# Kernel tuning notes

Hardware: AMD Instinct MI355X
Metric: run time of the kernel (lower is better)

Reference implementation:

```python
import jax, jax.numpy as jnp
import numpy as np

N_NODES = 50000
N_EDGES = 1600000
N_GRAPHS = 1000


def setup_inputs() -> dict:
    key = jax.random.key(0)
    ks = jax.random.split(key, 16)
    s = 0.1
    return {
        "x": jax.random.normal(ks[0], (N_NODES, 7), jnp.float32),
        "edge_attr": jax.random.normal(ks[1], (N_EDGES, 4), jnp.float32),
        "edge_index": jax.random.randint(ks[2], (2, N_EDGES), 0, N_NODES),
        "batch": jnp.sort(jax.random.randint(ks[3], (N_NODES,), 0, N_GRAPHS)),
        "We1": jax.random.normal(ks[4], (4, 7), jnp.float32) * s,
        "be1": jnp.zeros((7,), jnp.float32),
        "W1a": jax.random.normal(ks[5], (7, 64), jnp.float32) * s,
        "b1a": jnp.zeros((64,), jnp.float32),
        "W1b": jax.random.normal(ks[6], (64, 64), jnp.float32) * s,
        "b1b": jnp.zeros((64,), jnp.float32),
        "We2": jax.random.normal(ks[7], (4, 64), jnp.float32) * s,
        "be2": jnp.zeros((64,), jnp.float32),
        "W2a": jax.random.normal(ks[8], (64, 64), jnp.float32) * s,
        "b2a": jnp.zeros((64,), jnp.float32),
        "W2b": jax.random.normal(ks[9], (64, 64), jnp.float32) * s,
        "b2b": jnp.zeros((64,), jnp.float32),
        "Wfc": jax.random.normal(ks[10], (64, 12), jnp.float32) * s,
        "bfc": jnp.zeros((12,), jnp.float32),
    }


def _gine_conv(h, edge_attr, src, dst, We, be, Wa, ba, Wb, bb, n_nodes):
    # GINEConv (eps=0): out = nn(h + sum_j relu(h[src] + lin(edge_attr)))
    e = edge_attr @ We + be                      # [E, d]
    msg = jax.nn.relu(h[src] + e)                # [E, d] gather + add + relu
    aggr = jax.ops.segment_sum(msg, dst, num_segments=n_nodes)  # scatter-sum
    z = h + aggr
    return jax.nn.relu(z @ Wa + ba) @ Wb + bb


def reference(x, edge_attr, edge_index, batch,
              We1, be1, W1a, b1a, W1b, b1b,
              We2, be2, W2a, b2a, W2b, b2b,
              Wfc, bfc):
    src, dst = edge_index[0], edge_index[1]
    n = x.shape[0]
    h = jax.nn.relu(_gine_conv(x, edge_attr, src, dst, We1, be1, W1a, b1a, W1b, b1b, n))
    h = jax.nn.relu(_gine_conv(h, edge_attr, src, dst, We2, be2, W2a, b2a, W2b, b2b, n))
    # global mean pool over batch index
    sums = jax.ops.segment_sum(h, batch, num_segments=N_GRAPHS)          # [G, 64]
    cnt = jax.ops.segment_sum(jnp.ones((n,), h.dtype), batch, num_segments=N_GRAPHS)
    pooled = sums / jnp.maximum(cnt, 1.0)[:, None]
    return pooled @ Wfc + bfc                                            # [G, 12]
```

## Files before the change

kernel.cpp:

```cpp
#include <hip/hip_runtime.h>

typedef unsigned char uchar;
typedef unsigned short ushort;
typedef unsigned int uint;

constexpr int NN = 50000;
constexpr int NE = 1600000;
constexpr int NG = 1000;
constexpr int NB2 = 196;
constexpr int TILE = 4096;
constexpr int NTILE = (NE + TILE - 1) / TILE;
constexpr int SPAN_CAP = 9216;
constexpr int MSTRIDE = 72;

constexpr int OFF_BCNT  = 0;
constexpr int OFF_SUMS  = 256;
constexpr int OFF_CNT   = 64256;
constexpr int ZERO_UNITS= 65280;
constexpr int OFF_BBASE = 65280;
constexpr int OFF_BCUR  = 65536;
constexpr int OFF_OFFS  = 65792;
constexpr int OFF_P0    = 116224;
constexpr int OFF_P1    = 1716224;
constexpr int OFF_P2    = 3316224;
constexpr int OFF_Z1    = 4916224;
constexpr int OFF_H1    = 5316224;
constexpr int OFF_Z     = 6916224;

typedef __attribute__((ext_vector_type(8))) short short8;
typedef __attribute__((ext_vector_type(4))) float float4v;
typedef __attribute__((ext_vector_type(2))) float float2v;

__device__ __forceinline__ uint f2bf(float f) {
    uint u = __float_as_uint(f);
    return (u + 0x7fffu + ((u >> 16) & 1u)) >> 16;
}
__device__ __forceinline__ float bf2f_lo(uint p) { return __uint_as_float(p << 16); }
__device__ __forceinline__ float bf2f_hi(uint p) { return __uint_as_float(p & 0xffff0000u); }

__global__ __launch_bounds__(256) void bhist_kernel(const int* __restrict__ eidx,
                                                    int* __restrict__ bcnt) {
    __shared__ int lh[NB2];
    for (int i = threadIdx.x; i < NB2; i += 256) lh[i] = 0;
    __syncthreads();
    int tid = blockIdx.x * 256 + threadIdx.x;
    int stride = gridDim.x * 256;
    for (int e = tid; e < NE; e += stride) atomicAdd(&lh[eidx[NE + e] >> 8], 1);
    __syncthreads();
    for (int i = threadIdx.x; i < NB2; i += 256) if (lh[i]) atomicAdd(&bcnt[i], lh[i]);
}

__global__ __launch_bounds__(256) void bscan_kernel(const int* __restrict__ bcnt,
                                                    int* __restrict__ bbase,
                                                    int* __restrict__ bcur) {
    __shared__ int s[256];
    int t = threadIdx.x;
    int v = (t < NB2) ? bcnt[t] : 0;
    s[t] = v; __syncthreads();
    for (int o = 1; o < 256; o <<= 1) {
        int u = (t >= o) ? s[t - o] : 0;
        __syncthreads();
        s[t] += u;
        __syncthreads();
    }
    bbase[t] = s[t] - v;
    bcur[t] = s[t] - v;
}

__global__ __launch_bounds__(256) void bin_kernel(const int* __restrict__ eidx,
                                                  const float4* __restrict__ ea,
                                                  int* __restrict__ bcur,
                                                  uint* __restrict__ p0,
                                                  uint* __restrict__ p1,
                                                  uint* __restrict__ p2) {
    __shared__ uint s0[TILE], s1[TILE], s2[TILE];
    __shared__ int hcnt[NB2], hoff[NB2 + 1], hcur[NB2], gbase[NB2];
    const int t = threadIdx.x;
    const int e0 = blockIdx.x * TILE;
    const int cnt = (NE - e0 < TILE) ? (NE - e0) : TILE;
    for (int i = t; i < NB2; i += 256) hcnt[i] = 0;
    __syncthreads();
    int dsts[16];
    #pragma unroll
    for (int k = 0; k < 16; ++k) {
        int i = t + k * 256;
        int d = (i < cnt) ? eidx[NE + e0 + i] : -1;
        dsts[k] = d;
        if (d >= 0) atomicAdd(&hcnt[d >> 8], 1);
    }
    __syncthreads();
    if (t == 0) {
        int a = 0;
        for (int b = 0; b < NB2; ++b) { hoff[b] = a; a += hcnt[b]; }
        hoff[NB2] = a;
    }
    __syncthreads();
    if (t < NB2) { hcur[t] = hoff[t]; gbase[t] = atomicAdd(&bcur[t], hcnt[t]); }
    __syncthreads();
    #pragma unroll
    for (int k = 0; k < 16; ++k) {
        int d = dsts[k];
        if (d < 0) continue;
        int i = t + k * 256;
        int e = e0 + i;
        int src = eidx[e];
        float4 a = ea[e];
        int bkt = d >> 8;
        int lp = atomicAdd(&hcur[bkt], 1);
        s0[lp] = (uint)src | ((uint)(d & 255) << 16) | ((uint)bkt << 24);
        s1[lp] = f2bf(a.x) | (f2bf(a.y) << 16);
        s2[lp] = f2bf(a.z) | (f2bf(a.w) << 16);
    }
    __syncthreads();
    for (int i = t; i < cnt; i += 256) {
        uint r0 = s0[i];
        int bkt = (int)(r0 >> 24);
        int gp = gbase[bkt] + (i - hoff[bkt]);
        p0[gp] = r0; p1[gp] = s1[i]; p2[gp] = s2[i];
    }
}

__global__ __launch_bounds__(256) void build_kernel(const int* __restrict__ bbase,
                                                    const int* __restrict__ bcnt,
                                                    int* __restrict__ offs,
                                                    uint* __restrict__ p0,
                                                    uint* __restrict__ p1,
                                                    uint* __restrict__ p2) {
    __shared__ uint s0[SPAN_CAP], s1[SPAN_CAP], s2[SPAN_CAP];
    __shared__ int ldeg[256], lcur[256], sscan[256];
    const int t = threadIdx.x;
    const int b = blockIdx.x;
    const int nlo = b << 8;
    const int base = bbase[b];
    int span = bcnt[b];
    if (span > SPAN_CAP) span = SPAN_CAP;
    ldeg[t] = 0;
    __syncthreads();
    for (int i = t; i < span; i += 256)
        atomicAdd(&ldeg[(p0[base + i] >> 16) & 0xFFu], 1);
    __syncthreads();
    int v = ldeg[t];
    sscan[t] = v; __syncthreads();
    for (int o = 1; o < 256; o <<= 1) {
        int u = (t >= o) ? sscan[t - o] : 0;
        __syncthreads();
        sscan[t] += u;
        __syncthreads();
    }
    int exc = sscan[t] - v;
    lcur[t] = exc;
    int gi = nlo + t;
    if (gi < NN) offs[gi] = base + exc;
    else if (gi < 50176) offs[gi] = NE;
    __syncthreads();
    for (int i = t; i < span; i += 256) {
        uint r0 = p0[base + i], r1 = p1[base + i], r2 = p2[base + i];
        int pos = atomicAdd(&lcur[(r0 >> 16) & 0xFFu], 1);
        s0[pos] = r0; s1[pos] = r1; s2[pos] = r2;
    }
    __syncthreads();
    for (int i = t; i < span; i += 256) {
        p0[base + i] = s0[i]; p1[base + i] = s1[i]; p2[base + i] = s2[i];
    }
}

__global__ __launch_bounds__(256) void aggr1_kernel(
    const float* __restrict__ x,
    const uint* __restrict__ p0, const uint* __restrict__ p1, const uint* __restrict__ p2,
    const int* __restrict__ offs,
    const float* __restrict__ We1, const float* __restrict__ be1,
    float* __restrict__ z1)
{
    __shared__ float sWe[32];
    __shared__ float sbe[8];
    int tid = threadIdx.x;
    if (tid < 32) { int k = tid >> 3, dd = tid & 7; sWe[tid] = (dd < 7) ? We1[k * 7 + dd] : 0.f; }
    if (tid < 8)  sbe[tid] = (tid < 7) ? be1[tid] : 0.f;
    __syncthreads();

    const int w = tid >> 6, lane = tid & 63;
    const int jg = lane >> 3, d = lane & 7;

    for (int n = blockIdx.x * 4 + w; n < NN; n += gridDim.x * 4) {
        const int off = offs[n];
        const int deg = offs[n + 1] - off;
        float acc = 0.f;
        for (int j0 = 0; j0 < deg; j0 += 16) {
            int ja = j0 + jg;
            int jb = j0 + 8 + jg;
            int ia = off + ((ja < deg) ? ja : 0);
            int ib = off + ((jb < deg) ? jb : 0);
            uint r0a = p0[ia], r1a = p1[ia], r2a = p2[ia];
            uint r0b = p0[ib], r1b = p1[ib], r2b = p2[ib];
            float xa = (d < 7) ? x[(size_t)(r0a & 0xFFFFu) * 7 + d] : 0.f;
            float xb = (d < 7) ? x[(size_t)(r0b & 0xFFFFu) * 7 + d] : 0.f;
            float va = sbe[d] + bf2f_lo(r1a) * sWe[d] + bf2f_hi(r1a) * sWe[8 + d]
                     + bf2f_lo(r2a) * sWe[16 + d] + bf2f_hi(r2a) * sWe[24 + d] + xa;
            float vb = sbe[d] + bf2f_lo(r1b) * sWe[d] + bf2f_hi(r1b) * sWe[8 + d]
                     + bf2f_lo(r2b) * sWe[16 + d] + bf2f_hi(r2b) * sWe[24 + d] + xb;
            va = (d < 7 && ja < deg) ? fmaxf(va, 0.f) : 0.f;
            vb = (d < 7 && jb < deg) ? fmaxf(vb, 0.f) : 0.f;
            acc += va + vb;
        }
        acc += __shfl_xor(acc, 8);
        acc += __shfl_xor(acc, 16);
        acc += __shfl_xor(acc, 32);
        if (jg == 0)
            z1[(size_t)n * 8 + d] = (d < 7) ? (x[(size_t)n * 7 + d] + acc) : 0.f;
    }
}

__global__ __launch_bounds__(256) void node1_kernel(
    const float* __restrict__ z1,
    const float* __restrict__ W1a, const float* __restrict__ b1a,
    const float* __restrict__ W1b, const float* __restrict__ b1b,
    uint* __restrict__ h1u)
{
    __shared__ __align__(16) ushort sT[64 * MSTRIDE];
    __shared__ __align__(16) ushort sO[64 * 64];
    const int t = threadIdx.x;
    const int w = t >> 6, lane = t & 63;
    const int qm = lane & 15, quad = lane >> 4;
    const int n0 = blockIdx.x * 64;
    const int node = n0 + w * 16 + qm;

    short8 wa1n[4];
    #pragma unroll
    for (int nt = 0; nt < 4; ++nt) {
        short8 v = (short8)0;
        if (quad == 0) {
            #pragma unroll
            for (int j = 0; j < 7; ++j)
                v[j] = (short)f2bf(W1a[j * 64 + nt * 16 + qm]);
        }
        wa1n[nt] = v;
    }
    short8 wb1[2][4];
    #pragma unroll
    for (int s = 0; s < 2; ++s)
        #pragma unroll
        for (int nt = 0; nt < 4; ++nt) {
            short8 v;
            #pragma unroll
            for (int j = 0; j < 8; ++j)
                v[j] = (short)f2bf(W1b[(s * 32 + quad * 8 + j) * 64 + nt * 16 + qm]);
            wb1[s][nt] = v;
        }
    float ba[4], bb[4];
    #pragma unroll
    for (int nt = 0; nt < 4; ++nt) { ba[nt] = b1a[nt * 16 + qm]; bb[nt] = b1b[nt * 16 + qm]; }

    short8 af1 = (short8)0;
    if (quad == 0 && node < NN) {
        const float4 za = *(const float4*)(z1 + (size_t)node * 8);
        const float4 zbv = *(const float4*)(z1 + (size_t)node * 8 + 4);
        af1[0] = (short)f2bf(za.x); af1[1] = (short)f2bf(za.y);
        af1[2] = (short)f2bf(za.z); af1[3] = (short)f2bf(za.w);
        af1[4] = (short)f2bf(zbv.x); af1[5] = (short)f2bf(zbv.y);
        af1[6] = (short)f2bf(zbv.z); af1[7] = (short)f2bf(zbv.w);
    }
    float4v acc[4];
    #pragma unroll
    for (int nt = 0; nt < 4; ++nt) {
        acc[nt] = (float4v){0.f, 0.f, 0.f, 0.f};
        acc[nt] = __builtin_amdgcn_mfma_f32_16x16x32_bf16(af1, wa1n[nt], acc[nt], 0, 0, 0);
    }
    #pragma unroll
    for (int nt = 0; nt < 4; ++nt)
        #pragma unroll
        for (int r = 0; r < 4; ++r)
            sT[(w * 16 + quad * 4 + r) * MSTRIDE + nt * 16 + qm] =
                (ushort)f2bf(fmaxf(acc[nt][r] + ba[nt], 0.f));
    __syncthreads();

    #pragma unroll
    for (int nt = 0; nt < 4; ++nt) acc[nt] = (float4v){0.f, 0.f, 0.f, 0.f};
    #pragma unroll
    for (int s = 0; s < 2; ++s) {
        short8 af = *(const short8*)&sT[(w * 16 + qm) * MSTRIDE + s * 32 + quad * 8];
        #pragma unroll
        for (int nt = 0; nt < 4; ++nt)
            acc[nt] = __builtin_amdgcn_mfma_f32_16x16x32_bf16(af, wb1[s][nt], acc[nt], 0, 0, 0);
    }
    #pragma unroll
    for (int nt = 0; nt < 4; ++nt)
        #pragma unroll
        for (int r = 0; r < 4; ++r)
            sO[(w * 16 + quad * 4 + r) * 64 + nt * 16 + qm] =
                (ushort)f2bf(fmaxf(acc[nt][r] + bb[nt], 0.f));
    __syncthreads();
    for (int i = t; i < 64 * 32; i += 256) {
        int nd = i >> 5;
        if (n0 + nd < NN) h1u[(size_t)(n0 + nd) * 32 + (i & 31)] = ((const uint*)sO)[i];
    }
}

__global__ __launch_bounds__(256) void aggr2_kernel(
    const uint* __restrict__ h1u,
    const uint* __restrict__ p0, const uint* __restrict__ p1, const uint* __restrict__ p2,
    const int* __restrict__ offs,
    const float* __restrict__ We2, const float* __restrict__ be2,
    uint* __restrict__ zb)
{
    __shared__ float sWe[256];
    __shared__ float sbe[64];
    int tid = threadIdx.x;
    sWe[tid] = We2[tid];
    if (tid < 64) sbe[tid] = be2[tid];
    __syncthreads();
    const int w = tid >> 6, lane = tid & 63;
    const int l = lane & 31;
    const int half8 = (lane >> 5) << 3;
    const int n = blockIdx.x * 4 + w;
    const int off = offs[n];
    const int deg = offs[n + 1] - off;
    float2v w0v, w1v, w2v, w3v, bbv;
    w0v[0] = sWe[2 * l];       w0v[1] = sWe[2 * l + 1];
    w1v[0] = sWe[64 + 2 * l];  w1v[1] = sWe[64 + 2 * l + 1];
    w2v[0] = sWe[128 + 2 * l]; w2v[1] = sWe[128 + 2 * l + 1];
    w3v[0] = sWe[192 + 2 * l]; w3v[1] = sWe[192 + 2 * l + 1];
    bbv[0] = sbe[2 * l];       bbv[1] = sbe[2 * l + 1];
    const float2v zero2 = {0.f, 0.f};

    float2v accv = zero2;
    for (int jb = 0; jb < deg; jb += 16) {
        int m = deg - jb;
        int ll = (lane < 16) ? ((lane < m) ? lane : 0) : 0;
        int idx = off + jb + ll;
        int sx = (int)(p0[idx] & 0xFFFFu);
        uint e01 = p1[idx];
        uint e23 = p2[idx];
        uint g[8];
        #pragma unroll
        for (int k = 0; k < 8; ++k) {
            int mk = k + half8;
            int sk = __shfl(sx, (mk < m) ? mk : 0);
            g[k] = h1u[(size_t)sk * 32 + l];
        }
        #pragma unroll
        for (int k = 0; k < 8; ++k) {
            int mk = k + half8;
            int sl = (mk < m) ? mk : 0;
            uint py = (uint)__shfl((int)e01, sl);
            uint pz = (uint)__shfl((int)e23, sl);
            float2v bv = bbv + bf2f_lo(py) * w0v + bf2f_hi(py) * w1v
                       + bf2f_lo(pz) * w2v + bf2f_hi(pz) * w3v;
            float2v gv;
            gv[0] = bf2f_lo(g[k]);
            gv[1] = bf2f_hi(g[k]);
            float2v tv = gv + bv;
            tv[0] = fmaxf(tv[0], 0.f);
            tv[1] = fmaxf(tv[1], 0.f);
            if (mk < m) accv += tv;
        }
    }
    float accx = accv[0], accy = accv[1];
    accx += __shfl_xor(accx, 32);
    accy += __shfl_xor(accy, 32);
    if (lane < 32) {
        uint sw = h1u[(size_t)n * 32 + l];
        float zx = bf2f_lo(sw) + accx;
        float zy = bf2f_hi(sw) + accy;
        zb[(size_t)n * 32 + l] = f2bf(zx) | (f2bf(zy) << 16);
    }
}

__global__ __launch_bounds__(256) void mlp2_kernel(
    const uint* __restrict__ zb,
    const float* __restrict__ W2a, const float* __restrict__ b2a,
    const float* __restrict__ W2b, const float* __restrict__ b2b,
    const int* __restrict__ batch,
    float* __restrict__ sums, float* __restrict__ cnt)
{
    __shared__ __align__(16) ushort sT[64 * MSTRIDE];
    __shared__ float sH[64 * 64];
    __shared__ int sB[64];
    __shared__ float pbuf[4][64];
    __shared__ int pcnt[4];
    const int t = threadIdx.x;
    const int w = t >> 6, lane = t & 63;
    const int qm = lane & 15, quad = lane >> 4;
    const int n0 = blockIdx.x * 64;
    const int node = n0 + w * 16 + qm;
    const int nv = (NN - n0 < 64) ? (NN - n0) : 64;

    if (t < 64) sB[t] = (n0 + t < NN) ? batch[n0 + t] : -2;

    short8 wa[2][4], wb[2][4];
    #pragma unroll
    for (int s = 0; s < 2; ++s)
        #pragma unroll
        for (int nt = 0; nt < 4; ++nt) {
            short8 va, vb;
            #pragma unroll
            for (int j = 0; j < 8; ++j) {
                int k = s * 32 + quad * 8 + j, n = nt * 16 + qm;
                va[j] = (short)f2bf(W2a[k * 64 + n]);
                vb[j] = (short)f2bf(W2b[k * 64 + n]);
            }
            wa[s][nt] = va; wb[s][nt] = vb;
        }
    float ba[4], bb[4];
    #pragma unroll
    for (int nt = 0; nt < 4; ++nt) { ba[nt] = b2a[nt * 16 + qm]; bb[nt] = b2b[nt * 16 + qm]; }

    float4v acc[4];
    #pragma unroll
    for (int nt = 0; nt < 4; ++nt) acc[nt] = (float4v){0.f, 0.f, 0.f, 0.f};
    #pragma unroll
    for (int s = 0; s < 2; ++s) {
        uint4 zw = (node < NN) ? *(const uint4*)&zb[(size_t)node * 32 + s * 16 + quad * 4]
                               : make_uint4(0, 0, 0, 0);
        short8 af;
        *(uint4*)&af = zw;
        #pragma unroll
        for (int nt = 0; nt < 4; ++nt)
            acc[nt] = __builtin_amdgcn_mfma_f32_16x16x32_bf16(af, wa[s][nt], acc[nt], 0, 0, 0);
    }
    #pragma unroll
    for (int nt = 0; nt < 4; ++nt)
        #pragma unroll
        for (int r = 0; r < 4; ++r)
            sT[(w * 16 + quad * 4 + r) * MSTRIDE + nt * 16 + qm] =
                (ushort)f2bf(fmaxf(acc[nt][r] + ba[nt], 0.f));
    __syncthreads();

    #pragma unroll
    for (int nt = 0; nt < 4; ++nt) acc[nt] = (float4v){0.f, 0.f, 0.f, 0.f};
    #pragma unroll
    for (int s = 0; s < 2; ++s) {
        short8 af = *(const short8*)&sT[(w * 16 + qm) * MSTRIDE + s * 32 + quad * 8];
        #pragma unroll
        for (int nt = 0; nt < 4; ++nt)
            acc[nt] = __builtin_amdgcn_mfma_f32_16x16x32_bf16(af, wb[s][nt], acc[nt], 0, 0, 0);
    }
    #pragma unroll
    for (int nt = 0; nt < 4; ++nt)
        #pragma unroll
        for (int r = 0; r < 4; ++r)
            sH[(w * 16 + quad * 4 + r) * 64 + nt * 16 + qm] = fmaxf(acc[nt][r] + bb[nt], 0.f);
    __syncthreads();

    const int glo = sB[0];
    const int ghi = sB[nv - 1];
    const int c = t >> 6, d = t & 63;
    for (int g = glo; g <= ghi; ++g) {
        float p = 0.f;
        int lc = 0;
        #pragma unroll 4
        for (int i = 0; i < 16; ++i) {
            int nd = c * 16 + i;
            if (sB[nd] == g) { p += sH[nd * 64 + d]; ++lc; }
        }
        pbuf[c][d] = p;
        if (d == 0) pcnt[c] = lc;
        __syncthreads();
        int tc = pcnt[0] + pcnt[1] + pcnt[2] + pcnt[3];
        if (tc > 0) {
            if (c == 0) {
                float tot = pbuf[0][d] + pbuf[1][d] + pbuf[2][d] + pbuf[3][d];
                atomicAdd(&sums[(size_t)g * 64 + d], tot);
            }
            if (t == 0) atomicAdd(&cnt[g], (float)tc);
        }
        __syncthreads();
    }
}

__global__ __launch_bounds__(256) void fc_kernel(
    const float* __restrict__ sums, const float* __restrict__ cnt,
    const float* __restrict__ Wfc, const float* __restrict__ bfc,
    float* __restrict__ out)
{
    int gid = blockIdx.x * blockDim.x + threadIdx.x;
    if (gid >= NG * 12) return;
    int g = gid / 12, jj = gid - g * 12;
    float inv = 1.f / fmaxf(cnt[g], 1.f);
    float acc = bfc[jj];
    #pragma unroll 8
    for (int k = 0; k < 64; ++k) acc += sums[(size_t)g * 64 + k] * inv * Wfc[k * 12 + jj];
    out[gid] = acc;
}

extern "C" void kernel_launch(void* const* d_in, const int* in_sizes, int n_in,
                              void* d_out, int out_size, void* d_ws, size_t ws_size,
                              hipStream_t stream)
{
    (void)in_sizes; (void)n_in; (void)out_size; (void)ws_size;
    const float*  x    = (const float*)d_in[0];
    const float4* ea   = (const float4*)d_in[1];
    const int*    eidx = (const int*)d_in[2];
    const int*    batch= (const int*)d_in[3];
    const float*  We1  = (const float*)d_in[4];
    const float*  be1  = (const float*)d_in[5];
    const float*  W1a  = (const float*)d_in[6];
    const float*  b1a  = (const float*)d_in[7];
    const float*  W1b  = (const float*)d_in[8];
    const float*  b1b  = (const float*)d_in[9];
    const float*  We2  = (const float*)d_in[10];
    const float*  be2  = (const float*)d_in[11];
    const float*  W2a  = (const float*)d_in[12];
    const float*  b2a  = (const float*)d_in[13];
    const float*  W2b  = (const float*)d_in[14];
    const float*  b2b  = (const float*)d_in[15];
    const float*  Wfc  = (const float*)d_in[16];
    const float*  bfc  = (const float*)d_in[17];
    float* out = (float*)d_out;
    float* ws  = (float*)d_ws;

    int*   bcnt  = (int*)(ws + OFF_BCNT);
    float* sums  = ws + OFF_SUMS;
    float* cnt   = ws + OFF_CNT;
    int*   bbase = (int*)(ws + OFF_BBASE);
    int*   bcur  = (int*)(ws + OFF_BCUR);
    int*   offs  = (int*)(ws + OFF_OFFS);
    uint*  p0    = (uint*)(ws + OFF_P0);
    uint*  p1    = (uint*)(ws + OFF_P1);
    uint*  p2    = (uint*)(ws + OFF_P2);
    float* z1    = ws + OFF_Z1;
    uint*  h1u   = (uint*)(ws + OFF_H1);
    uint*  zb    = (uint*)(ws + OFF_Z);

    hipMemsetAsync(d_ws, 0, (size_t)ZERO_UNITS * 4, stream);

    bhist_kernel<<<256, 256, 0, stream>>>(eidx, bcnt);
    bscan_kernel<<<1, 256, 0, stream>>>(bcnt, bbase, bcur);
    bin_kernel  <<<NTILE, 256, 0, stream>>>(eidx, ea, bcur, p0, p1, p2);
    build_kernel<<<NB2, 256, 0, stream>>>(bbase, bcnt, offs, p0, p1, p2);
    aggr1_kernel<<<2500, 256, 0, stream>>>(x, p0, p1, p2, offs, We1, be1, z1);
    node1_kernel<<<(NN + 63) / 64, 256, 0, stream>>>(z1, W1a, b1a, W1b, b1b, h1u);
    aggr2_kernel<<<12500, 256, 0, stream>>>(h1u, p0, p1, p2, offs, We2, be2, zb);
    mlp2_kernel <<<(NN + 63) / 64, 256, 0, stream>>>(zb, W2a, b2a, W2b, b2b, batch, sums, cnt);
    fc_kernel   <<<(NG * 12 + 255) / 256, 256, 0, stream>>>(sums, cnt, Wfc, bfc, out);
}
```

Baseline: 280.0 us.

## Aggregate layer-2 edges per 32-node group with shared-memory atomics

The second aggregation kernel moves from one wavefront per destination node to one block per 32 consecutive nodes. Each half-wavefront handles an edge slot across the group's contiguous CSR edge range and accumulates into a shared-memory tile with atomic adds, using the dst low byte stored in p0. This removes the per-node degree-loop imbalance and the shuffle-heavy broadcast, which leaves lanes idle on low-degree nodes. In exchange it adds LDS atomic contention, depends on the packed dst-local field, and may index past offs when the last group is partial.

```diff
diff --git a/kernel.cpp b/kernel.cpp
--- a/kernel.cpp
+++ b/kernel.cpp
@@ -12,6 +12,8 @@
 constexpr int NTILE = (NE + TILE - 1) / TILE;
 constexpr int SPAN_CAP = 9216;
 constexpr int MSTRIDE = 72;
+constexpr int GRP = 32;
+constexpr int NGB = (NN + GRP - 1) / GRP;
 
 constexpr int OFF_BCNT  = 0;
 constexpr int OFF_SUMS  = 256;
@@ -304,64 +306,78 @@
 {
     __shared__ float sWe[256];
     __shared__ float sbe[64];
-    int tid = threadIdx.x;
+    __shared__ float sAcc[GRP][64];
+    const int tid = threadIdx.x;
     sWe[tid] = We2[tid];
     if (tid < 64) sbe[tid] = be2[tid];
-    __syncthreads();
-    const int w = tid >> 6, lane = tid & 63;
+    {
+        float* sa = &sAcc[0][0];
+        #pragma unroll
+        for (int i = tid; i < GRP * 64; i += 256) sa[i] = 0.f;
+    }
+    __syncthreads();
+
+    const int lane = tid & 63;
     const int l = lane & 31;
-    const int half8 = (lane >> 5) << 3;
-    const int n = blockIdx.x * 4 + w;
-    const int off = offs[n];
-    const int deg = offs[n + 1] - off;
+    const int hh = tid >> 5;
+    const int n0 = blockIdx.x * GRP;
+    const int estart = offs[n0];
+    const int eend = offs[n0 + GRP];
+    const int baseloc = n0 & 255;
+
     float2v w0v, w1v, w2v, w3v, bbv;
     w0v[0] = sWe[2 * l];       w0v[1] = sWe[2 * l + 1];
     w1v[0] = sWe[64 + 2 * l];  w1v[1] = sWe[64 + 2 * l + 1];
     w2v[0] = sWe[128 + 2 * l]; w2v[1] = sWe[128 + 2 * l + 1];
     w3v[0] = sWe[192 + 2 * l]; w3v[1] = sWe[192 + 2 * l + 1];
     bbv[0] = sbe[2 * l];       bbv[1] = sbe[2 * l + 1];
-    const float2v zero2 = {0.f, 0.f};
-
-    float2v accv = zero2;
-    for (int jb = 0; jb < deg; jb += 16) {
-        int m = deg - jb;
-        int ll = (lane < 16) ? ((lane < m) ? lane : 0) : 0;
-        int idx = off + jb + ll;
-        int sx = (int)(p0[idx] & 0xFFFFu);
-        uint e01 = p1[idx];
-        uint e23 = p2[idx];
-        uint g[8];
-        #pragma unroll
-        for (int k = 0; k < 8; ++k) {
-            int mk = k + half8;
-            int sk = __shfl(sx, (mk < m) ? mk : 0);
-            g[k] = h1u[(size_t)sk * 32 + l];
-        }
-        #pragma unroll
-        for (int k = 0; k < 8; ++k) {
-            int mk = k + half8;
-            int sl = (mk < m) ? mk : 0;
-            uint py = (uint)__shfl((int)e01, sl);
-            uint pz = (uint)__shfl((int)e23, sl);
-            float2v bv = bbv + bf2f_lo(py) * w0v + bf2f_hi(py) * w1v
-                       + bf2f_lo(pz) * w2v + bf2f_hi(pz) * w3v;
-            float2v gv;
-            gv[0] = bf2f_lo(g[k]);
-            gv[1] = bf2f_hi(g[k]);
-            float2v tv = gv + bv;
-            tv[0] = fmaxf(tv[0], 0.f);
-            tv[1] = fmaxf(tv[1], 0.f);
-            if (mk < m) accv += tv;
-        }
-    }
-    float accx = accv[0], accy = accv[1];
-    accx += __shfl_xor(accx, 32);
-    accy += __shfl_xor(accy, 32);
-    if (lane < 32) {
-        uint sw = h1u[(size_t)n * 32 + l];
-        float zx = bf2f_lo(sw) + accx;
-        float zy = bf2f_hi(sw) + accy;
-        zb[(size_t)n * 32 + l] = f2bf(zx) | (f2bf(zy) << 16);
+
+    int e = estart + hh;
+    for (; e + 24 < eend; e += 32) {
+        uint r0[4], ry[4], rz[4];
+        #pragma unroll
+        for (int k = 0; k < 4; ++k) {
+            r0[k] = p0[e + 8 * k];
+            ry[k] = p1[e + 8 * k];
+            rz[k] = p2[e + 8 * k];
+        }
+        uint g[4];
+        #pragma unroll
+        for (int k = 0; k < 4; ++k)
+            g[k] = h1u[((r0[k] & 0xFFFFu) << 5) + l];
+        #pragma unroll
+        for (int k = 0; k < 4; ++k) {
+            float2v bv = bbv + bf2f_lo(ry[k]) * w0v + bf2f_hi(ry[k]) * w1v
+                       + bf2f_lo(rz[k]) * w2v + bf2f_hi(rz[k]) * w3v;
+            float t0 = fmaxf(bf2f_lo(g[k]) + bv[0], 0.f);
+            float t1 = fmaxf(bf2f_hi(g[k]) + bv[1], 0.f);
+            int loc = (int)((r0[k] >> 16) & 0xFFu) - baseloc;
+            atomicAdd(&sAcc[loc][l], t0);
+            atomicAdd(&sAcc[loc][32 + l], t1);
+        }
+    }
+    for (; e < eend; e += 8) {
+        uint r0 = p0[e], ry = p1[e], rz = p2[e];
+        uint g = h1u[((r0 & 0xFFFFu) << 5) + l];
+        float2v bv = bbv + bf2f_lo(ry) * w0v + bf2f_hi(ry) * w1v
+                   + bf2f_lo(rz) * w2v + bf2f_hi(rz) * w3v;
+        float t0 = fmaxf(bf2f_lo(g) + bv[0], 0.f);
+        float t1 = fmaxf(bf2f_hi(g) + bv[1], 0.f);
+        int loc = (int)((r0 >> 16) & 0xFFu) - baseloc;
+        atomicAdd(&sAcc[loc][l], t0);
+        atomicAdd(&sAcc[loc][32 + l], t1);
+    }
+    __syncthreads();
+
+    for (int i = tid; i < GRP * 32; i += 256) {
+        int ndl = i >> 5, c = i & 31;
+        int nd = n0 + ndl;
+        if (nd < NN) {
+            uint sw = h1u[(size_t)nd * 32 + c];
+            float zx = bf2f_lo(sw) + sAcc[ndl][c];
+            float zy = bf2f_hi(sw) + sAcc[ndl][32 + c];
+            zb[(size_t)nd * 32 + c] = f2bf(zx) | (f2bf(zy) << 16);
+        }
     }
 }
 
@@ -529,7 +545,7 @@
     build_kernel<<<NB2, 256, 0, stream>>>(bbase, bcnt, offs, p0, p1, p2);
     aggr1_kernel<<<2500, 256, 0, stream>>>(x, p0, p1, p2, offs, We1, be1, z1);
     node1_kernel<<<(NN + 63) / 64, 256, 0, stream>>>(z1, W1a, b1a, W1b, b1b, h1u);
-    aggr2_kernel<<<12500, 256, 0, stream>>>(h1u, p0, p1, p2, offs, We2, be2, zb);
+    aggr2_kernel<<<NGB, 256, 0, stream>>>(h1u, p0, p1, p2, offs, We2, be2, zb);
     mlp2_kernel <<<(NN + 63) / 64, 256, 0, stream>>>(zb, W2a, b2a, W2b, b2b, batch, sums, cnt);
     fc_kernel   <<<(NG * 12 + 255) / 256, 256, 0, stream>>>(sums, cnt, Wfc, bfc, out);
 }
```

New measurement: 823.3 us. +194.0%, slower.

## Remap aggr2 to four nodes per wavefront with 16-lane groups and uint2 gathers

Applied to the files above, without the earlier changes.

Layer-2 aggregation now gives each 16-lane group its own destination node, so one wavefront handles four nodes instead of one. Each lane covers four features through 8-byte gathers, edges are processed two at a time, and the edge-weight vectors are loaded straight from global memory rather than staged in shared memory. This removes the shuffle broadcasts, the shared-memory barrier and the 16-edge batch padding. In exchange, every group loops to the largest degree among the four nodes in its wave, and each lane issues its own edge-record loads, which are redundant across the group.

```diff
diff --git a/kernel.cpp b/kernel.cpp
--- a/kernel.cpp
+++ b/kernel.cpp
@@ -12,6 +12,8 @@
 constexpr int NTILE = (NE + TILE - 1) / TILE;
 constexpr int SPAN_CAP = 9216;
 constexpr int MSTRIDE = 72;
+constexpr int NPB = 16;
+constexpr int NBLK2 = NN / NPB;
 
 constexpr int OFF_BCNT  = 0;
 constexpr int OFF_SUMS  = 256;
@@ -302,67 +304,95 @@
     const float* __restrict__ We2, const float* __restrict__ be2,
     uint* __restrict__ zb)
 {
-    __shared__ float sWe[256];
-    __shared__ float sbe[64];
-    int tid = threadIdx.x;
-    sWe[tid] = We2[tid];
-    if (tid < 64) sbe[tid] = be2[tid];
-    __syncthreads();
-    const int w = tid >> 6, lane = tid & 63;
-    const int l = lane & 31;
-    const int half8 = (lane >> 5) << 3;
-    const int n = blockIdx.x * 4 + w;
+    const int tid = threadIdx.x;
+    const int lane = tid & 63;
+    const int wv = tid >> 6;
+    const int grp = lane >> 4;
+    const int cl = lane & 15;
+    const int n = blockIdx.x * NPB + wv * 4 + grp;
+
+    float2v wA[4], wB[4], bA, bB;
+    #pragma unroll
+    for (int k = 0; k < 4; ++k) {
+        const float4 w4 = *(const float4*)&We2[k * 64 + 4 * cl];
+        wA[k][0] = w4.x; wA[k][1] = w4.y;
+        wB[k][0] = w4.z; wB[k][1] = w4.w;
+    }
+    {
+        const float4 b4 = *(const float4*)&be2[4 * cl];
+        bA[0] = b4.x; bA[1] = b4.y;
+        bB[0] = b4.z; bB[1] = b4.w;
+    }
+
     const int off = offs[n];
     const int deg = offs[n + 1] - off;
-    float2v w0v, w1v, w2v, w3v, bbv;
-    w0v[0] = sWe[2 * l];       w0v[1] = sWe[2 * l + 1];
-    w1v[0] = sWe[64 + 2 * l];  w1v[1] = sWe[64 + 2 * l + 1];
-    w2v[0] = sWe[128 + 2 * l]; w2v[1] = sWe[128 + 2 * l + 1];
-    w3v[0] = sWe[192 + 2 * l]; w3v[1] = sWe[192 + 2 * l + 1];
-    bbv[0] = sbe[2 * l];       bbv[1] = sbe[2 * l + 1];
+    const int degm1 = (deg > 0) ? deg - 1 : 0;
+    const int offC = (deg > 0) ? off : 0;
+    int dmax = deg;
+    dmax = max(dmax, __shfl_xor(dmax, 16));
+    dmax = max(dmax, __shfl_xor(dmax, 32));
+
+    float2v accA = {0.f, 0.f}, accB = {0.f, 0.f};
     const float2v zero2 = {0.f, 0.f};
-
-    float2v accv = zero2;
-    for (int jb = 0; jb < deg; jb += 16) {
-        int m = deg - jb;
-        int ll = (lane < 16) ? ((lane < m) ? lane : 0) : 0;
-        int idx = off + jb + ll;
-        int sx = (int)(p0[idx] & 0xFFFFu);
-        uint e01 = p1[idx];
-        uint e23 = p2[idx];
-        uint g[8];
-        #pragma unroll
-        for (int k = 0; k < 8; ++k) {
-            int mk = k + half8;
-            int sk = __shfl(sx, (mk < m) ? mk : 0);
-            g[k] = h1u[(size_t)sk * 32 + l];
-        }
-        #pragma unroll
-        for (int k = 0; k < 8; ++k) {
-            int mk = k + half8;
-            int sl = (mk < m) ? mk : 0;
-            uint py = (uint)__shfl((int)e01, sl);
-            uint pz = (uint)__shfl((int)e23, sl);
-            float2v bv = bbv + bf2f_lo(py) * w0v + bf2f_hi(py) * w1v
-                       + bf2f_lo(pz) * w2v + bf2f_hi(pz) * w3v;
-            float2v gv;
-            gv[0] = bf2f_lo(g[k]);
-            gv[1] = bf2f_hi(g[k]);
-            float2v tv = gv + bv;
-            tv[0] = fmaxf(tv[0], 0.f);
-            tv[1] = fmaxf(tv[1], 0.f);
-            if (mk < m) accv += tv;
-        }
-    }
-    float accx = accv[0], accy = accv[1];
-    accx += __shfl_xor(accx, 32);
-    accy += __shfl_xor(accy, 32);
-    if (lane < 32) {
-        uint sw = h1u[(size_t)n * 32 + l];
-        float zx = bf2f_lo(sw) + accx;
-        float zy = bf2f_hi(sw) + accy;
-        zb[(size_t)n * 32 + l] = f2bf(zx) | (f2bf(zy) << 16);
-    }
+    int j = 0;
+    for (; j + 2 <= dmax; j += 2) {
+        const bool q0 = (j < deg), q1 = (j + 1 < deg);
+        const int e0 = offC + (q0 ? j : degm1);
+        const int e1 = offC + (q1 ? j + 1 : degm1);
+        const uint r00 = p0[e0], ry0 = p1[e0], rz0 = p2[e0];
+        const uint r01 = p0[e1], ry1 = p1[e1], rz1 = p2[e1];
+        const uint2 g0 = *(const uint2*)&h1u[((size_t)(r00 & 0xFFFFu) << 5) + 2 * cl];
+        const uint2 g1 = *(const uint2*)&h1u[((size_t)(r01 & 0xFFFFu) << 5) + 2 * cl];
+        {
+            float2v bvA = bA + bf2f_lo(ry0) * wA[0] + bf2f_hi(ry0) * wA[1]
+                        + bf2f_lo(rz0) * wA[2] + bf2f_hi(rz0) * wA[3];
+            float2v bvB = bB + bf2f_lo(ry0) * wB[0] + bf2f_hi(ry0) * wB[1]
+                        + bf2f_lo(rz0) * wB[2] + bf2f_hi(rz0) * wB[3];
+            float2v tA, tB;
+            tA[0] = fmaxf(bf2f_lo(g0.x) + bvA[0], 0.f);
+            tA[1] = fmaxf(bf2f_hi(g0.x) + bvA[1], 0.f);
+            tB[0] = fmaxf(bf2f_lo(g0.y) + bvB[0], 0.f);
+            tB[1] = fmaxf(bf2f_hi(g0.y) + bvB[1], 0.f);
+            accA += q0 ? tA : zero2;
+            accB += q0 ? tB : zero2;
+        }
+        {
+            float2v bvA = bA + bf2f_lo(ry1) * wA[0] + bf2f_hi(ry1) * wA[1]
+                        + bf2f_lo(rz1) * wA[2] + bf2f_hi(rz1) * wA[3];
+            float2v bvB = bB + bf2f_lo(ry1) * wB[0] + bf2f_hi(ry1) * wB[1]
+                        + bf2f_lo(rz1) * wB[2] + bf2f_hi(rz1) * wB[3];
+            float2v tA, tB;
+            tA[0] = fmaxf(bf2f_lo(g1.x) + bvA[0], 0.f);
+            tA[1] = fmaxf(bf2f_hi(g1.x) + bvA[1], 0.f);
+            tB[0] = fmaxf(bf2f_lo(g1.y) + bvB[0], 0.f);
+            tB[1] = fmaxf(bf2f_hi(g1.y) + bvB[1], 0.f);
+            accA += q1 ? tA : zero2;
+            accB += q1 ? tB : zero2;
+        }
+    }
+    if (j < dmax) {
+        const bool q0 = (j < deg);
+        const int e0 = offC + (q0 ? j : degm1);
+        const uint r00 = p0[e0], ry0 = p1[e0], rz0 = p2[e0];
+        const uint2 g0 = *(const uint2*)&h1u[((size_t)(r00 & 0xFFFFu) << 5) + 2 * cl];
+        float2v bvA = bA + bf2f_lo(ry0) * wA[0] + bf2f_hi(ry0) * wA[1]
+                    + bf2f_lo(rz0) * wA[2] + bf2f_hi(rz0) * wA[3];
+        float2v bvB = bB + bf2f_lo(ry0) * wB[0] + bf2f_hi(ry0) * wB[1]
+                    + bf2f_lo(rz0) * wB[2] + bf2f_hi(rz0) * wB[3];
+        float2v tA, tB;
+        tA[0] = fmaxf(bf2f_lo(g0.x) + bvA[0], 0.f);
+        tA[1] = fmaxf(bf2f_hi(g0.x) + bvA[1], 0.f);
+        tB[0] = fmaxf(bf2f_lo(g0.y) + bvB[0], 0.f);
+        tB[1] = fmaxf(bf2f_hi(g0.y) + bvB[1], 0.f);
+        accA += q0 ? tA : zero2;
+        accB += q0 ? tB : zero2;
+    }
+
+    const uint2 hw = *(const uint2*)&h1u[(size_t)n * 32 + 2 * cl];
+    uint o0 = f2bf(bf2f_lo(hw.x) + accA[0]) | (f2bf(bf2f_hi(hw.x) + accA[1]) << 16);
+    uint o1 = f2bf(bf2f_lo(hw.y) + accB[0]) | (f2bf(bf2f_hi(hw.y) + accB[1]) << 16);
+    uint2 ov; ov.x = o0; ov.y = o1;
+    *(uint2*)&zb[(size_t)n * 32 + 2 * cl] = ov;
 }
 
 __global__ __launch_bounds__(256) void mlp2_kernel(
@@ -529,7 +559,7 @@
     build_kernel<<<NB2, 256, 0, stream>>>(bbase, bcnt, offs, p0, p1, p2);
     aggr1_kernel<<<2500, 256, 0, stream>>>(x, p0, p1, p2, offs, We1, be1, z1);
     node1_kernel<<<(NN + 63) / 64, 256, 0, stream>>>(z1, W1a, b1a, W1b, b1b, h1u);
-    aggr2_kernel<<<12500, 256, 0, stream>>>(h1u, p0, p1, p2, offs, We2, be2, zb);
+    aggr2_kernel<<<NBLK2, 256, 0, stream>>>(h1u, p0, p1, p2, offs, We2, be2, zb);
     mlp2_kernel <<<(NN + 63) / 64, 256, 0, stream>>>(zb, W2a, b2a, W2b, b2b, batch, sums, cnt);
     fc_kernel   <<<(NG * 12 + 255) / 256, 256, 0, stream>>>(sums, cnt, Wfc, bfc, out);
 }
```

Result: no change. 275.1 us (-1.7%).
